# Optimization experiments

Hardware: AMD Instinct MI355X
Metric: run time of the kernel (lower is better)

Reference implementation:

```python
import jax, jax.numpy as jnp
import numpy as np


def setup_inputs() -> dict:
    key = jax.random.key(0)
    kq, kk, kv = jax.random.split(key, 3)
    B, L, H, E = 4, 2048, 16, 64
    return {
        "queries": jax.random.normal(kq, (B, L, H, E), dtype=jnp.float32),
        "keys": jax.random.normal(kk, (B, L, H, E), dtype=jnp.float32),
        "values": jax.random.normal(kv, (B, L, H, E), dtype=jnp.float32),
    }


def reference(queries, keys, values):
    # queries: [B,L,H,E], keys: [B,S,H,E], values: [B,S,H,D]
    B, L, H, E = queries.shape
    S = keys.shape[1]
    scale = 1.0 / jnp.sqrt(jnp.asarray(E, dtype=queries.dtype))
    scores = jnp.einsum("blhe,bshe->bhls", queries, keys)  # [B,H,L,S]
    # causal mask: block strictly-upper-triangular (future) positions
    causal = jnp.tril(jnp.ones((L, S), dtype=bool))  # True = keep
    scores = jnp.where(causal[None, None, :, :], scores, -jnp.inf)
    A = jax.nn.softmax(scale * scores, axis=-1)  # dropout p=0 -> identity
    V = jnp.einsum("bhls,bshd->blhd", A, values)
    return V
```

## Files before the change

kernel.cpp:

```cpp
#include <hip/hip_runtime.h>
#include <hip/hip_bf16.h>

typedef float f32x4 __attribute__((ext_vector_type(4)));
typedef __bf16 bf16x8 __attribute__((ext_vector_type(8)));
typedef unsigned short u16x8 __attribute__((ext_vector_type(8)));
typedef unsigned u32x4 __attribute__((ext_vector_type(4)));

#define NB 4
#define SL 2048
#define NH 16
#define HD 64
#define KBLK 64
#define PAD 72
#define NT 16

static __device__ __forceinline__ unsigned short f2bf(float f) {
    unsigned u = __builtin_bit_cast(unsigned, f);
    u += 0x7fffu + ((u >> 16) & 1u);
    return (unsigned short)(u >> 16);
}

static __device__ __forceinline__ unsigned pk2(float lo, float hi) {
    unsigned r;
    asm("v_cvt_pk_bf16_f32 %0, %1, %2" : "=v"(r) : "v"(lo), "v"(hi));
    return r;
}

static __device__ __forceinline__ float fexp2(float x) {
    float r;
    asm("v_exp_f32 %0, %1" : "=v"(r) : "v"(x));
    return r;
}

static __device__ __forceinline__ void pl32swap(unsigned& a, unsigned& b) {
    asm("v_permlane32_swap_b32 %0, %1" : "+v"(a), "+v"(b));
}
static __device__ __forceinline__ void pl16swap(unsigned& a, unsigned& b) {
    asm("v_permlane16_swap_b32 %0, %1" : "+v"(a), "+v"(b));
}

__global__ void conv_v(const float* __restrict__ Vg, unsigned short* __restrict__ Vtb) {
    __shared__ unsigned short T[64 * PAD];
    const int tid = threadIdx.x;
    const int id  = blockIdx.x;
    const int st  = id & 31;
    const int bh  = id >> 5;
    const int s0  = st * 64;
    {
        const int sl = tid >> 2, c = (tid & 3) * 16;
        const float* src = Vg + ((size_t)((bh >> 4) * SL + s0 + sl) * NH + (bh & 15)) * HD + c;
        u16x8 a, b2;
        #pragma unroll
        for (int j = 0; j < 8; ++j) { a[j] = f2bf(src[j]); b2[j] = f2bf(src[8 + j]); }
        *(u16x8*)&T[sl * PAD + c]     = a;
        *(u16x8*)&T[sl * PAD + c + 8] = b2;
    }
    __syncthreads();
    {
        const int d = tid >> 2, sc = (tid & 3) * 16;
        u16x8 o0, o1;
        #pragma unroll
        for (int j = 0; j < 8; ++j) { o0[j] = T[(sc + j) * PAD + d]; o1[j] = T[(sc + 8 + j) * PAD + d]; }
        unsigned short* dst = Vtb + ((size_t)bh * HD + d) * SL + s0 + sc;
        *(u16x8*)dst       = o0;
        *(u16x8*)(dst + 8) = o1;
    }
}

__global__ __launch_bounds__(256, 2)
void fattn_kernel(const float* __restrict__ Qg, const float* __restrict__ Kg,
                  const unsigned short* __restrict__ Vtb, float* __restrict__ Og)
{
    __shared__ unsigned short Klds[KBLK * PAD];
    __shared__ unsigned short Vlds[HD * PAD];

    const int tid  = threadIdx.x;
    const int w    = tid >> 6;
    const int lane = tid & 63;
    const int g    = lane >> 4;
    const int li   = lane & 15;

    const int bh   = blockIdx.x & 63;
    const int rawp = blockIdx.x >> 6;
    const int p    = (rawp < 4) ? rawp : 11 - rawp;
    const int b    = bh >> 4;
    const int h    = bh & 15;

    const float QSCALE = 0.125f * 1.44269504088896f;
    const int srow = tid >> 2;
    const int scol = (tid & 3) * 16;
    const float* kgbase = Kg + ((size_t)b * SL * NH + h) * HD;
    const unsigned short* vbase = Vtb + (size_t)bh * HD * SL;

    #pragma unroll 1
    for (int phase = 0; phase < 2; ++phase) {
        const int tile = (phase == 0) ? (NT - 1 - p) : p;
        const int tmax = 2 * tile + 1;

        int qrows[2];
        qrows[0] = tile * 128 + w * 16;
        qrows[1] = tile * 128 + 64 + w * 16;

        bf16x8 qfrag[2][2];
        #pragma unroll
        for (int fi = 0; fi < 2; ++fi) {
            const int q = qrows[fi] + li;
            const float* qp = Qg + ((size_t)(b * SL + q) * NH + h) * HD + g * 8;
            #pragma unroll
            for (int c = 0; c < 2; ++c) {
                f32x4 a = *(const f32x4*)(qp + c * 32);
                f32x4 b2 = *(const f32x4*)(qp + c * 32 + 4);
                u16x8 t;
                #pragma unroll
                for (int j = 0; j < 4; ++j) { t[j] = f2bf(a[j] * QSCALE); t[4 + j] = f2bf(b2[j] * QSCALE); }
                qfrag[fi][c] = __builtin_bit_cast(bf16x8, t);
            }
        }

        float m_run[2] = {-1e30f, -1e30f};
        float l_run[2] = {0.f, 0.f};
        f32x4 oacc[2][4];
        #pragma unroll
        for (int fi = 0; fi < 2; ++fi)
            #pragma unroll
            for (int d = 0; d < 4; ++d) oacc[fi][d] = f32x4{0.f, 0.f, 0.f, 0.f};

        f32x4 kf[4];
        #pragma unroll
        for (int j = 0; j < 4; ++j)
            kf[j] = *(const f32x4*)(kgbase + (size_t)srow * NH * HD + scol + j * 4);
        u16x8 vr0 = *(const u16x8*)(vbase + (size_t)srow * SL + scol);
        u16x8 vr1 = *(const u16x8*)(vbase + (size_t)srow * SL + scol + 8);

        for (int t = 0; t <= tmax; ++t) {
            const int s0 = t * KBLK;
            __syncthreads();
            {
                u32x4 a0 = {pk2(kf[0][0], kf[0][1]), pk2(kf[0][2], kf[0][3]),
                            pk2(kf[1][0], kf[1][1]), pk2(kf[1][2], kf[1][3])};
                u32x4 a1 = {pk2(kf[2][0], kf[2][1]), pk2(kf[2][2], kf[2][3]),
                            pk2(kf[3][0], kf[3][1]), pk2(kf[3][2], kf[3][3])};
                *(u16x8*)&Klds[srow * PAD + scol]     = __builtin_bit_cast(u16x8, a0);
                *(u16x8*)&Klds[srow * PAD + scol + 8] = __builtin_bit_cast(u16x8, a1);
                *(u16x8*)&Vlds[srow * PAD + scol]     = vr0;
                *(u16x8*)&Vlds[srow * PAD + scol + 8] = vr1;
            }
            {
                const int s1 = (t < tmax) ? (s0 + KBLK) : 0;
                const bool doPf = (t < tmax) || (phase == 0);
                if (doPf) {
                    #pragma unroll
                    for (int j = 0; j < 4; ++j)
                        kf[j] = *(const f32x4*)(kgbase + (size_t)(s1 + srow) * NH * HD + scol + j * 4);
                    vr0 = *(const u16x8*)(vbase + (size_t)srow * SL + s1 + scol);
                    vr1 = *(const u16x8*)(vbase + (size_t)srow * SL + s1 + scol + 8);
                }
            }
            __syncthreads();

            bool act[2];
            #pragma unroll
            for (int fi = 0; fi < 2; ++fi) act[fi] = (s0 <= qrows[fi] + 15);

            bf16x8 kfr[4][2];
            #pragma unroll
            for (int sub = 0; sub < 4; ++sub) {
                kfr[sub][0] = __builtin_bit_cast(bf16x8, *(u16x8*)&Klds[(sub * 16 + li) * PAD + g * 8]);
                kfr[sub][1] = __builtin_bit_cast(bf16x8, *(u16x8*)&Klds[(sub * 16 + li) * PAD + 32 + g * 8]);
            }

            bf16x8 pfr[2][2];
            #pragma unroll
            for (int fi = 0; fi < 2; ++fi) {
                if (!act[fi]) continue;
                const int qf = qrows[fi];

                f32x4 sacc[4];
                #pragma unroll
                for (int sub = 0; sub < 4; ++sub) {
                    f32x4 c = f32x4{0.f, 0.f, 0.f, 0.f};
                    c = __builtin_amdgcn_mfma_f32_16x16x32_bf16(kfr[sub][0], qfrag[fi][0], c, 0, 0, 0);
                    c = __builtin_amdgcn_mfma_f32_16x16x32_bf16(kfr[sub][1], qfrag[fi][1], c, 0, 0, 0);
                    sacc[sub] = c;
                }

                if (s0 + KBLK - 1 > qf) {
                    const int q = qf + li;
                    #pragma unroll
                    for (int sub = 0; sub < 4; ++sub)
                        #pragma unroll
                        for (int r = 0; r < 4; ++r)
                            if (s0 + sub * 16 + g * 4 + r > q) sacc[sub][r] = -1e30f;
                }

                float a0 = fmaxf(sacc[0][0], sacc[0][1]), a1 = fmaxf(sacc[0][2], sacc[0][3]);
                float a2 = fmaxf(sacc[1][0], sacc[1][1]), a3 = fmaxf(sacc[1][2], sacc[1][3]);
                float a4 = fmaxf(sacc[2][0], sacc[2][1]), a5 = fmaxf(sacc[2][2], sacc[2][3]);
                float a6 = fmaxf(sacc[3][0], sacc[3][1]), a7 = fmaxf(sacc[3][2], sacc[3][3]);
                float b0 = fmaxf(a0, a1), b1 = fmaxf(a2, a3), b2 = fmaxf(a4, a5), b3 = fmaxf(a6, a7);
                float pp = fmaxf(fmaxf(b0, b1), fmaxf(b2, b3));

                if (!__all(pp - m_run[fi] <= 8.0f)) {
                    float pmax = pp;
                    pmax = fmaxf(pmax, __shfl_xor(pmax, 16, 64));
                    pmax = fmaxf(pmax, __shfl_xor(pmax, 32, 64));
                    const float mnew = fmaxf(m_run[fi], pmax);
                    const float alpha = fexp2(m_run[fi] - mnew);
                    m_run[fi] = mnew;
                    l_run[fi] *= alpha;
                    #pragma unroll
                    for (int d = 0; d < 4; ++d)
                        #pragma unroll
                        for (int r = 0; r < 4; ++r) oacc[fi][d][r] *= alpha;
                }

                #pragma unroll
                for (int sub = 0; sub < 4; ++sub)
                    #pragma unroll
                    for (int r = 0; r < 4; ++r)
                        sacc[sub][r] = fexp2(sacc[sub][r] - m_run[fi]);
                float s0a = (sacc[0][0] + sacc[0][1]) + (sacc[0][2] + sacc[0][3]);
                float s1a = (sacc[1][0] + sacc[1][1]) + (sacc[1][2] + sacc[1][3]);
                float s2a = (sacc[2][0] + sacc[2][1]) + (sacc[2][2] + sacc[2][3]);
                float s3a = (sacc[3][0] + sacc[3][1]) + (sacc[3][2] + sacc[3][3]);
                l_run[fi] += (s0a + s1a) + (s2a + s3a);

                unsigned X00 = pk2(sacc[0][0], sacc[0][1]);
                unsigned X01 = pk2(sacc[0][2], sacc[0][3]);
                unsigned X10 = pk2(sacc[1][0], sacc[1][1]);
                unsigned X11 = pk2(sacc[1][2], sacc[1][3]);
                unsigned X20 = pk2(sacc[2][0], sacc[2][1]);
                unsigned X21 = pk2(sacc[2][2], sacc[2][3]);
                unsigned X30 = pk2(sacc[3][0], sacc[3][1]);
                unsigned X31 = pk2(sacc[3][2], sacc[3][3]);
                pl32swap(X00, X10); pl16swap(X00, X10);
                pl32swap(X01, X11); pl16swap(X01, X11);
                pl32swap(X20, X30); pl16swap(X20, X30);
                pl32swap(X21, X31); pl16swap(X21, X31);
                u32x4 w0 = {X00, X01, X10, X11};
                u32x4 w1 = {X20, X21, X30, X31};
                pfr[fi][0] = __builtin_bit_cast(bf16x8, w0);
                pfr[fi][1] = __builtin_bit_cast(bf16x8, w1);
            }

            #pragma unroll
            for (int d = 0; d < 4; ++d) {
                bf16x8 vf0 = __builtin_bit_cast(bf16x8, *(u16x8*)&Vlds[(d * 16 + li) * PAD + g * 8]);
                bf16x8 vf1 = __builtin_bit_cast(bf16x8, *(u16x8*)&Vlds[(d * 16 + li) * PAD + 32 + g * 8]);
                #pragma unroll
                for (int fi = 0; fi < 2; ++fi) {
                    if (!act[fi]) continue;
                    oacc[fi][d] = __builtin_amdgcn_mfma_f32_16x16x32_bf16(vf0, pfr[fi][0], oacc[fi][d], 0, 0, 0);
                    oacc[fi][d] = __builtin_amdgcn_mfma_f32_16x16x32_bf16(vf1, pfr[fi][1], oacc[fi][d], 0, 0, 0);
                }
            }
        }

        #pragma unroll
        for (int fi = 0; fi < 2; ++fi) {
            float lt = l_run[fi];
            lt += __shfl_xor(lt, 16, 64);
            lt += __shfl_xor(lt, 32, 64);
            const float inv = 1.0f / lt;
            float* op = Og + ((size_t)(b * SL + qrows[fi] + li) * NH + h) * HD + g * 4;
            #pragma unroll
            for (int d = 0; d < 4; ++d) {
                f32x4 o = oacc[fi][d];
                #pragma unroll
                for (int r = 0; r < 4; ++r) o[r] *= inv;
                *(f32x4*)(op + d * 16) = o;
            }
        }
    }
}

extern "C" void kernel_launch(void* const* d_in, const int* in_sizes, int n_in,
                              void* d_out, int out_size, void* d_ws, size_t ws_size,
                              hipStream_t stream) {
    const float* Qg = (const float*)d_in[0];
    const float* Kg = (const float*)d_in[1];
    const float* Vg = (const float*)d_in[2];
    float* Og = (float*)d_out;

    const size_t elems = (size_t)NB * NH * SL * HD;
    if (ws_size < elems * sizeof(unsigned short)) return;
    unsigned short* Vtb = (unsigned short*)d_ws;

    hipLaunchKernelGGL(conv_v, dim3(NB * NH * (SL / 64)), dim3(256), 0, stream, Vg, Vtb);
    hipLaunchKernelGGL(fattn_kernel, dim3(8 * 64), dim3(256), 0, stream,
                       Qg, Kg, Vtb, Og);
}
```

Before: 77.57 us.

## Switch to 32x32x16 MFMA and pair short/long query tiles in one pass

Replaces the 16x16x32 bf16 MFMA tiles with 32x32x16 MFMA tiles. Each wave now owns 32 query rows, and the P fragments are rebuilt with a single permlane32 swap. The two-phase loop over a long and a short causal tile is merged into one K/V sweep. In that sweep each wave handles one row block from tile p and one from tile NT-1-p, so K/V tiles are loaded once and shared by both. This is meant to cut K/V reloads and fragment shuffle overhead, and the larger MFMA should run more efficiently. In exchange it uses more accumulator registers, which may hurt occupancy, and the row-max and row-sum reductions per lane get longer.

```diff
diff --git a/kernel.cpp b/kernel.cpp
--- a/kernel.cpp
+++ b/kernel.cpp
@@ -2,6 +2,7 @@
 #include <hip/hip_bf16.h>
 
 typedef float f32x4 __attribute__((ext_vector_type(4)));
+typedef float f32x16 __attribute__((ext_vector_type(16)));
 typedef __bf16 bf16x8 __attribute__((ext_vector_type(8)));
 typedef unsigned short u16x8 __attribute__((ext_vector_type(8)));
 typedef unsigned u32x4 __attribute__((ext_vector_type(4)));
@@ -34,9 +35,6 @@
 
 static __device__ __forceinline__ void pl32swap(unsigned& a, unsigned& b) {
     asm("v_permlane32_swap_b32 %0, %1" : "+v"(a), "+v"(b));
-}
-static __device__ __forceinline__ void pl16swap(unsigned& a, unsigned& b) {
-    asm("v_permlane16_swap_b32 %0, %1" : "+v"(a), "+v"(b));
 }
 
 __global__ void conv_v(const float* __restrict__ Vg, unsigned short* __restrict__ Vtb) {
@@ -77,8 +75,8 @@
     const int tid  = threadIdx.x;
     const int w    = tid >> 6;
     const int lane = tid & 63;
-    const int g    = lane >> 4;
-    const int li   = lane & 15;
+    const int l31  = lane & 31;
+    const int hi   = lane >> 5;
 
     const int bh   = blockIdx.x & 63;
     const int rawp = blockIdx.x >> 6;
@@ -86,191 +84,211 @@
     const int b    = bh >> 4;
     const int h    = bh & 15;
 
+    int qrows[2];
+    qrows[0] = p * 128 + w * 32;
+    qrows[1] = (NT - 1 - p) * 128 + w * 32;
+    const int tmax = 2 * (NT - 1 - p) + 1;
+
     const float QSCALE = 0.125f * 1.44269504088896f;
+    bf16x8 qfrag[2][4];
+    #pragma unroll
+    for (int fi = 0; fi < 2; ++fi) {
+        const int q = qrows[fi] + l31;
+        const float* qp = Qg + ((size_t)(b * SL + q) * NH + h) * HD + hi * 8;
+        #pragma unroll
+        for (int kk = 0; kk < 4; ++kk) {
+            f32x4 a = *(const f32x4*)(qp + kk * 16);
+            f32x4 b2 = *(const f32x4*)(qp + kk * 16 + 4);
+            u16x8 t;
+            #pragma unroll
+            for (int j = 0; j < 4; ++j) { t[j] = f2bf(a[j] * QSCALE); t[4 + j] = f2bf(b2[j] * QSCALE); }
+            qfrag[fi][kk] = __builtin_bit_cast(bf16x8, t);
+        }
+    }
+
+    float m_run[2] = {-1e30f, -1e30f};
+    float l_run[2] = {0.f, 0.f};
+    f32x16 oacc[2][2];
+    #pragma unroll
+    for (int fi = 0; fi < 2; ++fi)
+        #pragma unroll
+        for (int d = 0; d < 2; ++d)
+            #pragma unroll
+            for (int r = 0; r < 16; ++r) oacc[fi][d][r] = 0.f;
+
     const int srow = tid >> 2;
     const int scol = (tid & 3) * 16;
     const float* kgbase = Kg + ((size_t)b * SL * NH + h) * HD;
     const unsigned short* vbase = Vtb + (size_t)bh * HD * SL;
 
-    #pragma unroll 1
-    for (int phase = 0; phase < 2; ++phase) {
-        const int tile = (phase == 0) ? (NT - 1 - p) : p;
-        const int tmax = 2 * tile + 1;
-
-        int qrows[2];
-        qrows[0] = tile * 128 + w * 16;
-        qrows[1] = tile * 128 + 64 + w * 16;
-
-        bf16x8 qfrag[2][2];
+    f32x4 kf[4];
+    #pragma unroll
+    for (int j = 0; j < 4; ++j)
+        kf[j] = *(const f32x4*)(kgbase + (size_t)srow * NH * HD + scol + j * 4);
+    u16x8 vr0 = *(const u16x8*)(vbase + (size_t)srow * SL + scol);
+    u16x8 vr1 = *(const u16x8*)(vbase + (size_t)srow * SL + scol + 8);
+
+    for (int t = 0; t <= tmax; ++t) {
+        const int s0 = t * KBLK;
+        __syncthreads();
+        {
+            u32x4 a0 = {pk2(kf[0][0], kf[0][1]), pk2(kf[0][2], kf[0][3]),
+                        pk2(kf[1][0], kf[1][1]), pk2(kf[1][2], kf[1][3])};
+            u32x4 a1 = {pk2(kf[2][0], kf[2][1]), pk2(kf[2][2], kf[2][3]),
+                        pk2(kf[3][0], kf[3][1]), pk2(kf[3][2], kf[3][3])};
+            *(u16x8*)&Klds[srow * PAD + scol]     = __builtin_bit_cast(u16x8, a0);
+            *(u16x8*)&Klds[srow * PAD + scol + 8] = __builtin_bit_cast(u16x8, a1);
+            *(u16x8*)&Vlds[srow * PAD + scol]     = vr0;
+            *(u16x8*)&Vlds[srow * PAD + scol + 8] = vr1;
+        }
+        if (t < tmax) {
+            const int s1 = s0 + KBLK;
+            #pragma unroll
+            for (int j = 0; j < 4; ++j)
+                kf[j] = *(const f32x4*)(kgbase + (size_t)(s1 + srow) * NH * HD + scol + j * 4);
+            vr0 = *(const u16x8*)(vbase + (size_t)srow * SL + s1 + scol);
+            vr1 = *(const u16x8*)(vbase + (size_t)srow * SL + s1 + scol + 8);
+        }
+        __syncthreads();
+
+        bool act[2];
+        #pragma unroll
+        for (int fi = 0; fi < 2; ++fi) act[fi] = (s0 <= qrows[fi] + 31);
+
+        bf16x8 kfr[2][4];
+        #pragma unroll
+        for (int ms = 0; ms < 2; ++ms)
+            #pragma unroll
+            for (int kk = 0; kk < 4; ++kk)
+                kfr[ms][kk] = __builtin_bit_cast(bf16x8,
+                    *(u16x8*)&Klds[(ms * 32 + l31) * PAD + kk * 16 + hi * 8]);
+
+        bf16x8 pfr[2][4];
         #pragma unroll
         for (int fi = 0; fi < 2; ++fi) {
-            const int q = qrows[fi] + li;
-            const float* qp = Qg + ((size_t)(b * SL + q) * NH + h) * HD + g * 8;
-            #pragma unroll
-            for (int c = 0; c < 2; ++c) {
-                f32x4 a = *(const f32x4*)(qp + c * 32);
-                f32x4 b2 = *(const f32x4*)(qp + c * 32 + 4);
-                u16x8 t;
-                #pragma unroll
-                for (int j = 0; j < 4; ++j) { t[j] = f2bf(a[j] * QSCALE); t[4 + j] = f2bf(b2[j] * QSCALE); }
-                qfrag[fi][c] = __builtin_bit_cast(bf16x8, t);
-            }
-        }
-
-        float m_run[2] = {-1e30f, -1e30f};
-        float l_run[2] = {0.f, 0.f};
-        f32x4 oacc[2][4];
-        #pragma unroll
-        for (int fi = 0; fi < 2; ++fi)
-            #pragma unroll
-            for (int d = 0; d < 4; ++d) oacc[fi][d] = f32x4{0.f, 0.f, 0.f, 0.f};
-
-        f32x4 kf[4];
-        #pragma unroll
-        for (int j = 0; j < 4; ++j)
-            kf[j] = *(const f32x4*)(kgbase + (size_t)srow * NH * HD + scol + j * 4);
-        u16x8 vr0 = *(const u16x8*)(vbase + (size_t)srow * SL + scol);
-        u16x8 vr1 = *(const u16x8*)(vbase + (size_t)srow * SL + scol + 8);
-
-        for (int t = 0; t <= tmax; ++t) {
-            const int s0 = t * KBLK;
-            __syncthreads();
+            if (!act[fi]) continue;
+            const int qf = qrows[fi];
+
+            f32x16 sacc[2];
+            #pragma unroll
+            for (int ms = 0; ms < 2; ++ms) {
+                f32x16 c;
+                #pragma unroll
+                for (int r = 0; r < 16; ++r) c[r] = 0.f;
+                #pragma unroll
+                for (int kk = 0; kk < 4; ++kk)
+                    c = __builtin_amdgcn_mfma_f32_32x32x16_bf16(kfr[ms][kk], qfrag[fi][kk], c, 0, 0, 0);
+                sacc[ms] = c;
+            }
+
+            if (s0 + KBLK - 1 > qf) {
+                const int q = qf + l31;
+                #pragma unroll
+                for (int ms = 0; ms < 2; ++ms)
+                    #pragma unroll
+                    for (int r = 0; r < 16; ++r) {
+                        const int s = s0 + ms * 32 + (r & 3) + 8 * (r >> 2) + 4 * hi;
+                        if (s > q) sacc[ms][r] = -1e30f;
+                    }
+            }
+
+            float u[16];
+            #pragma unroll
+            for (int i = 0; i < 8; ++i) u[i]     = fmaxf(sacc[0][2 * i], sacc[0][2 * i + 1]);
+            #pragma unroll
+            for (int i = 0; i < 8; ++i) u[8 + i] = fmaxf(sacc[1][2 * i], sacc[1][2 * i + 1]);
+            #pragma unroll
+            for (int st = 8; st >= 1; st >>= 1)
+                #pragma unroll
+                for (int i = 0; i < 16; ++i)
+                    if (i < st) u[i] = fmaxf(u[i], u[i + st]);
+            const float pp = u[0];
+
+            if (!__all(pp - m_run[fi] <= 8.0f)) {
+                float pmax = fmaxf(pp, __shfl_xor(pp, 32, 64));
+                const float mnew = fmaxf(m_run[fi], pmax);
+                const float alpha = fexp2(m_run[fi] - mnew);
+                m_run[fi] = mnew;
+                l_run[fi] *= alpha;
+                #pragma unroll
+                for (int d = 0; d < 2; ++d)
+                    #pragma unroll
+                    for (int r = 0; r < 16; ++r) oacc[fi][d][r] *= alpha;
+            }
+
+            #pragma unroll
+            for (int ms = 0; ms < 2; ++ms)
+                #pragma unroll
+                for (int r = 0; r < 16; ++r)
+                    sacc[ms][r] = fexp2(sacc[ms][r] - m_run[fi]);
             {
-                u32x4 a0 = {pk2(kf[0][0], kf[0][1]), pk2(kf[0][2], kf[0][3]),
-                            pk2(kf[1][0], kf[1][1]), pk2(kf[1][2], kf[1][3])};
-                u32x4 a1 = {pk2(kf[2][0], kf[2][1]), pk2(kf[2][2], kf[2][3]),
-                            pk2(kf[3][0], kf[3][1]), pk2(kf[3][2], kf[3][3])};
-                *(u16x8*)&Klds[srow * PAD + scol]     = __builtin_bit_cast(u16x8, a0);
-                *(u16x8*)&Klds[srow * PAD + scol + 8] = __builtin_bit_cast(u16x8, a1);
-                *(u16x8*)&Vlds[srow * PAD + scol]     = vr0;
-                *(u16x8*)&Vlds[srow * PAD + scol + 8] = vr1;
-            }
-            {
-                const int s1 = (t < tmax) ? (s0 + KBLK) : 0;
-                const bool doPf = (t < tmax) || (phase == 0);
-                if (doPf) {
+                float sv[16];
+                #pragma unroll
+                for (int i = 0; i < 8; ++i) sv[i]     = sacc[0][2 * i] + sacc[0][2 * i + 1];
+                #pragma unroll
+                for (int i = 0; i < 8; ++i) sv[8 + i] = sacc[1][2 * i] + sacc[1][2 * i + 1];
+                #pragma unroll
+                for (int st = 8; st >= 1; st >>= 1)
                     #pragma unroll
-                    for (int j = 0; j < 4; ++j)
-                        kf[j] = *(const f32x4*)(kgbase + (size_t)(s1 + srow) * NH * HD + scol + j * 4);
-                    vr0 = *(const u16x8*)(vbase + (size_t)srow * SL + s1 + scol);
-                    vr1 = *(const u16x8*)(vbase + (size_t)srow * SL + s1 + scol + 8);
+                    for (int i = 0; i < 16; ++i)
+                        if (i < st) sv[i] += sv[i + st];
+                l_run[fi] += sv[0];
+            }
+
+            #pragma unroll
+            for (int ms = 0; ms < 2; ++ms) {
+                unsigned Y0[4], Y1[4];
+                #pragma unroll
+                for (int k = 0; k < 4; ++k) {
+                    Y0[k] = pk2(sacc[ms][4 * k + 0], sacc[ms][4 * k + 1]);
+                    Y1[k] = pk2(sacc[ms][4 * k + 2], sacc[ms][4 * k + 3]);
                 }
-            }
-            __syncthreads();
-
-            bool act[2];
-            #pragma unroll
-            for (int fi = 0; fi < 2; ++fi) act[fi] = (s0 <= qrows[fi] + 15);
-
-            bf16x8 kfr[4][2];
-            #pragma unroll
-            for (int sub = 0; sub < 4; ++sub) {
-                kfr[sub][0] = __builtin_bit_cast(bf16x8, *(u16x8*)&Klds[(sub * 16 + li) * PAD + g * 8]);
-                kfr[sub][1] = __builtin_bit_cast(bf16x8, *(u16x8*)&Klds[(sub * 16 + li) * PAD + 32 + g * 8]);
-            }
-
-            bf16x8 pfr[2][2];
+                #pragma unroll
+                for (int c = 0; c < 2; ++c) {
+                    unsigned X0 = Y0[2 * c], Z0 = Y0[2 * c + 1];
+                    unsigned X1 = Y1[2 * c], Z1 = Y1[2 * c + 1];
+                    pl32swap(X0, Z0);
+                    pl32swap(X1, Z1);
+                    u32x4 wv = {X0, X1, Z0, Z1};
+                    pfr[fi][ms * 2 + c] = __builtin_bit_cast(bf16x8, wv);
+                }
+            }
+        }
+
+        #pragma unroll
+        for (int dsub = 0; dsub < 2; ++dsub) {
+            bf16x8 vf[4];
+            #pragma unroll
+            for (int sc = 0; sc < 4; ++sc)
+                vf[sc] = __builtin_bit_cast(bf16x8,
+                    *(u16x8*)&Vlds[(dsub * 32 + l31) * PAD + sc * 16 + hi * 8]);
             #pragma unroll
             for (int fi = 0; fi < 2; ++fi) {
                 if (!act[fi]) continue;
-                const int qf = qrows[fi];
-
-                f32x4 sacc[4];
-                #pragma unroll
-                for (int sub = 0; sub < 4; ++sub) {
-                    f32x4 c = f32x4{0.f, 0.f, 0.f, 0.f};
-                    c = __builtin_amdgcn_mfma_f32_16x16x32_bf16(kfr[sub][0], qfrag[fi][0], c, 0, 0, 0);
-                    c = __builtin_amdgcn_mfma_f32_16x16x32_bf16(kfr[sub][1], qfrag[fi][1], c, 0, 0, 0);
-                    sacc[sub] = c;
-                }
-
-                if (s0 + KBLK - 1 > qf) {
-                    const int q = qf + li;
-                    #pragma unroll
-                    for (int sub = 0; sub < 4; ++sub)
-                        #pragma unroll
-                        for (int r = 0; r < 4; ++r)
-                            if (s0 + sub * 16 + g * 4 + r > q) sacc[sub][r] = -1e30f;
-                }
-
-                float a0 = fmaxf(sacc[0][0], sacc[0][1]), a1 = fmaxf(sacc[0][2], sacc[0][3]);
-                float a2 = fmaxf(sacc[1][0], sacc[1][1]), a3 = fmaxf(sacc[1][2], sacc[1][3]);
-                float a4 = fmaxf(sacc[2][0], sacc[2][1]), a5 = fmaxf(sacc[2][2], sacc[2][3]);
-                float a6 = fmaxf(sacc[3][0], sacc[3][1]), a7 = fmaxf(sacc[3][2], sacc[3][3]);
-                float b0 = fmaxf(a0, a1), b1 = fmaxf(a2, a3), b2 = fmaxf(a4, a5), b3 = fmaxf(a6, a7);
-                float pp = fmaxf(fmaxf(b0, b1), fmaxf(b2, b3));
-
-                if (!__all(pp - m_run[fi] <= 8.0f)) {
-                    float pmax = pp;
-                    pmax = fmaxf(pmax, __shfl_xor(pmax, 16, 64));
-                    pmax = fmaxf(pmax, __shfl_xor(pmax, 32, 64));
-                    const float mnew = fmaxf(m_run[fi], pmax);
-                    const float alpha = fexp2(m_run[fi] - mnew);
-                    m_run[fi] = mnew;
-                    l_run[fi] *= alpha;
-                    #pragma unroll
-                    for (int d = 0; d < 4; ++d)
-                        #pragma unroll
-                        for (int r = 0; r < 4; ++r) oacc[fi][d][r] *= alpha;
-                }
-
-                #pragma unroll
-                for (int sub = 0; sub < 4; ++sub)
-                    #pragma unroll
-                    for (int r = 0; r < 4; ++r)
-                        sacc[sub][r] = fexp2(sacc[sub][r] - m_run[fi]);
-                float s0a = (sacc[0][0] + sacc[0][1]) + (sacc[0][2] + sacc[0][3]);
-                float s1a = (sacc[1][0] + sacc[1][1]) + (sacc[1][2] + sacc[1][3]);
-                float s2a = (sacc[2][0] + sacc[2][1]) + (sacc[2][2] + sacc[2][3]);
-                float s3a = (sacc[3][0] + sacc[3][1]) + (sacc[3][2] + sacc[3][3]);
-                l_run[fi] += (s0a + s1a) + (s2a + s3a);
-
-                unsigned X00 = pk2(sacc[0][0], sacc[0][1]);
-                unsigned X01 = pk2(sacc[0][2], sacc[0][3]);
-                unsigned X10 = pk2(sacc[1][0], sacc[1][1]);
-                unsigned X11 = pk2(sacc[1][2], sacc[1][3]);
-                unsigned X20 = pk2(sacc[2][0], sacc[2][1]);
-                unsigned X21 = pk2(sacc[2][2], sacc[2][3]);
-                unsigned X30 = pk2(sacc[3][0], sacc[3][1]);
-                unsigned X31 = pk2(sacc[3][2], sacc[3][3]);
-                pl32swap(X00, X10); pl16swap(X00, X10);
-                pl32swap(X01, X11); pl16swap(X01, X11);
-                pl32swap(X20, X30); pl16swap(X20, X30);
-                pl32swap(X21, X31); pl16swap(X21, X31);
-                u32x4 w0 = {X00, X01, X10, X11};
-                u32x4 w1 = {X20, X21, X30, X31};
-                pfr[fi][0] = __builtin_bit_cast(bf16x8, w0);
-                pfr[fi][1] = __builtin_bit_cast(bf16x8, w1);
-            }
-
-            #pragma unroll
-            for (int d = 0; d < 4; ++d) {
-                bf16x8 vf0 = __builtin_bit_cast(bf16x8, *(u16x8*)&Vlds[(d * 16 + li) * PAD + g * 8]);
-                bf16x8 vf1 = __builtin_bit_cast(bf16x8, *(u16x8*)&Vlds[(d * 16 + li) * PAD + 32 + g * 8]);
-                #pragma unroll
-                for (int fi = 0; fi < 2; ++fi) {
-                    if (!act[fi]) continue;
-                    oacc[fi][d] = __builtin_amdgcn_mfma_f32_16x16x32_bf16(vf0, pfr[fi][0], oacc[fi][d], 0, 0, 0);
-                    oacc[fi][d] = __builtin_amdgcn_mfma_f32_16x16x32_bf16(vf1, pfr[fi][1], oacc[fi][d], 0, 0, 0);
-                }
-            }
-        }
-
-        #pragma unroll
-        for (int fi = 0; fi < 2; ++fi) {
-            float lt = l_run[fi];
-            lt += __shfl_xor(lt, 16, 64);
-            lt += __shfl_xor(lt, 32, 64);
-            const float inv = 1.0f / lt;
-            float* op = Og + ((size_t)(b * SL + qrows[fi] + li) * NH + h) * HD + g * 4;
-            #pragma unroll
-            for (int d = 0; d < 4; ++d) {
-                f32x4 o = oacc[fi][d];
-                #pragma unroll
-                for (int r = 0; r < 4; ++r) o[r] *= inv;
-                *(f32x4*)(op + d * 16) = o;
-            }
-        }
+                #pragma unroll
+                for (int sc = 0; sc < 4; ++sc)
+                    oacc[fi][dsub] = __builtin_amdgcn_mfma_f32_32x32x16_bf16(
+                        vf[sc], pfr[fi][sc], oacc[fi][dsub], 0, 0, 0);
+            }
+        }
+    }
+
+    #pragma unroll
+    for (int fi = 0; fi < 2; ++fi) {
+        float lt = l_run[fi];
+        lt += __shfl_xor(lt, 32, 64);
+        const float inv = 1.0f / lt;
+        float* op = Og + ((size_t)(b * SL + qrows[fi] + l31) * NH + h) * HD + 4 * hi;
+        #pragma unroll
+        for (int dsub = 0; dsub < 2; ++dsub)
+            #pragma unroll
+            for (int q2 = 0; q2 < 4; ++q2) {
+                f32x4 o = {oacc[fi][dsub][4 * q2 + 0] * inv,
+                           oacc[fi][dsub][4 * q2 + 1] * inv,
+                           oacc[fi][dsub][4 * q2 + 2] * inv,
+                           oacc[fi][dsub][4 * q2 + 3] * inv};
+                *(f32x4*)(op + dsub * 32 + 8 * q2) = o;
+            }
     }
 }
 
```

Result: faster. 74.63 us, median of 2 (-3.8%).
